# Optimization experiments

Measured on AMD Instinct MI355X. Metric: run time of the kernel, lower is better.

Reference implementation:

```python
import jax, jax.numpy as jnp
import numpy as np

B, C = 2, 128
FMAP_HW = [(256, 256), (128, 128), (64, 64), (32, 32)]
N_ROIS = 4000
POOL = (7, 7)
N_ANCH = 300000
N_POS = 1000          # anchors with match > 0 (class 1)
N_NEG = 200000        # anchors with match == -1
SHEM_POOLSIZE = 20
N_CLASSES = 2


def setup_inputs() -> dict:
    key = jax.random.key(0)
    ks = jax.random.split(key, 10)
    inp = {}
    for l, (h, w) in enumerate(FMAP_HW):
        inp[f"fmap{l}"] = jax.random.normal(ks[l], (B, C, h, w), dtype=jnp.float32)
    # rois: normalized (y1, x1, y2, x2, batch_ix)
    ctr = jax.random.uniform(ks[4], (N_ROIS, 2))
    sz = jax.random.uniform(ks[5], (N_ROIS, 2), minval=0.02, maxval=0.5)
    lo = jnp.clip(ctr - sz / 2, 0.0, 1.0)
    hi = jnp.clip(ctr + sz / 2, 0.0, 1.0)
    bix = jax.random.randint(ks[6], (N_ROIS, 1), 0, B).astype(jnp.float32)
    inp["rois"] = jnp.concatenate([lo, hi, bix], axis=1)
    # fixed layout for static shapes: [pos | neg | neutral]
    am = np.zeros(N_ANCH, np.int32)
    am[:N_POS] = 1
    am[N_POS:N_POS + N_NEG] = -1
    inp["anchor_matches"] = jnp.asarray(am)
    inp["class_pred_logits"] = jax.random.normal(ks[7], (N_ANCH, N_CLASSES), dtype=jnp.float32)
    inp["pred_deltas"] = jax.random.normal(ks[8], (N_ANCH, 4), dtype=jnp.float32) * 0.1
    inp["target_deltas"] = jax.random.normal(ks[9], (N_ANCH, 4), dtype=jnp.float32) * 0.1
    return inp


def _roi_align_2d(fmap, boxes, batch_ix, pool):
    """Bilinear ROI align, one sample at each bin center.
    fmap: [B,C,H,W]; boxes: [N,4] in fmap pixel coords (y1,x1,y2,x2).
    Returns [N,C,ph,pw]."""
    Hc, Wc = fmap.shape[2], fmap.shape[3]
    ph, pw = pool
    y1, x1, y2, x2 = boxes[:, 0], boxes[:, 1], boxes[:, 2], boxes[:, 3]
    bh = (y2 - y1) / ph
    bw = (x2 - x1) / pw
    iy = jnp.arange(ph, dtype=jnp.float32) + 0.5
    ix = jnp.arange(pw, dtype=jnp.float32) + 0.5
    sy = jnp.clip(y1[:, None] + bh[:, None] * iy[None, :], 0.0, Hc - 1.0)  # [N,ph]
    sx = jnp.clip(x1[:, None] + bw[:, None] * ix[None, :], 0.0, Wc - 1.0)  # [N,pw]
    y0f = jnp.floor(sy)
    x0f = jnp.floor(sx)
    y0 = y0f.astype(jnp.int32)
    x0 = x0f.astype(jnp.int32)
    y1i = jnp.minimum(y0 + 1, Hc - 1)
    x1i = jnp.minimum(x0 + 1, Wc - 1)
    wy = (sy - y0f)[:, :, None, None]  # [N,ph,1,1]
    wx = (sx - x0f)[:, None, :, None]  # [N,1,pw,1]
    b = batch_ix[:, None, None]

    def gather(yy, xx):
        # yy [N,ph], xx [N,pw] -> [N,ph,pw,C]
        return fmap[b, :, yy[:, :, None], xx[:, None, :]]

    v00 = gather(y0, x0)
    v01 = gather(y0, x1i)
    v10 = gather(y1i, x0)
    v11 = gather(y1i, x1i)
    out = (v00 * (1 - wy) * (1 - wx) + v01 * (1 - wy) * wx
           + v10 * wy * (1 - wx) + v11 * wy * wx)
    return jnp.transpose(out, (0, 3, 1, 2))


def _forward(fmaps, rois, anchor_matches, class_pred_logits, pred_deltas, target_deltas):
    boxes = rois[:, :4]
    batch_ix = rois[:, 4].astype(jnp.int32)
    h = boxes[:, 2] - boxes[:, 0]
    w = boxes[:, 3] - boxes[:, 1]
    roi_level = jnp.clip(
        jnp.round(4.0 + jnp.log2(jnp.sqrt(h * w + 1e-12))).astype(jnp.int32), 0, 3)
    boxes_sg = jax.lax.stop_gradient(boxes)  # original detaches level_boxes
    pooled = jnp.zeros((N_ROIS, C, POOL[0], POOL[1]), fmaps[0].dtype)
    for lvl, f in enumerate(fmaps):
        He, We = f.shape[2], f.shape[3]
        lb = boxes_sg * jnp.array([He, We, He, We], jnp.float32)
        pl = _roi_align_2d(f, lb, batch_ix, POOL)
        mask = (roi_level == lvl).astype(pl.dtype)[:, None, None, None]
        pooled = pooled + mask * pl  # each roi hits exactly one level; order preserved

    # ---- class loss with SHEM (layout: [:N_POS] pos, [N_POS:N_POS+N_NEG] neg) ----
    pos_logits = class_pred_logits[:N_POS]
    pos_targets = anchor_matches[:N_POS].astype(jnp.int32)
    pos_logp = jax.nn.log_softmax(pos_logits, axis=1)
    pos_loss = -jnp.mean(jnp.take_along_axis(pos_logp, pos_targets[:, None], axis=1))

    neg_logits = class_pred_logits[N_POS:N_POS + N_NEG]
    neg_bg_prob = jax.nn.softmax(neg_logits, axis=1)[:, 0]
    negative_count = N_POS  # max(1, n_pos)
    pool_n = min(negative_count * SHEM_POOLSIZE, N_NEG)
    order = jnp.argsort(neg_bg_prob)          # ascending bg prob = hardest first
    pool_idx = order[:pool_n]
    perm = jax.random.permutation(jax.random.key(1), pool_n)
    neg_ix = pool_idx[perm[:negative_count]]  # stochastic draw from hard pool
    neg_loss = -jnp.mean(jax.nn.log_softmax(neg_logits[neg_ix], axis=1)[:, 0])
    class_loss = (pos_loss + neg_loss) / 2.0

    # ---- bbox smooth-L1 on positives (beta=1, mean reduction) ----
    diff = jnp.abs(pred_deltas[:N_POS] - target_deltas[:N_POS])
    sl1 = jnp.where(diff < 1.0, 0.5 * diff * diff, diff - 0.5)
    bbox_loss = jnp.mean(sl1)
    return pooled, class_loss, bbox_loss


def reference(fmap0, fmap1, fmap2, fmap3, rois, anchor_matches,
              class_pred_logits, pred_deltas, target_deltas):
    return _forward([fmap0, fmap1, fmap2, fmap3], rois, anchor_matches,
                    class_pred_logits, pred_deltas, target_deltas)
```

## Files before the change

kernel.cpp:

```cpp
#include <hip/hip_runtime.h>
#include <hip/hip_bf16.h>
#include <cstdint>

#define NROIS  4000
#define NCH    128
#define NBINS  49
#define N_POSA 1000
#define N_NEGA 200000
#define POOLN  20000
#define HBITS_A 13
#define ABINS  8192
#define PBINS  4096
#define SUBN   4096
#define NTRBLK 2720
#define NPREP  106
#define NRANKA 512
#define NRANKP 40
#define TPAD   136

#define L0OFF 0ull
#define L1OFF 16777216ull
#define L2OFF 20971520ull
#define L3OFF 22020096ull
#define TLELEMS 22282240ull

__device__ __forceinline__ uint32_t rotl32d(uint32_t v, int r) { return (v << r) | (v >> (32-r)); }

__device__ void tf2x32(uint32_t k0, uint32_t k1, uint32_t& x0, uint32_t& x1)
{
    const uint32_t ks2 = k0 ^ k1 ^ 0x1BD11BDAu;
    const int R0[4] = {13,15,26,6};
    const int R1[4] = {17,29,16,24};
    x0 += k0; x1 += k1;
#pragma unroll
    for (int r = 0; r < 4; ++r) { x0 += x1; x1 = rotl32d(x1, R0[r]); x1 ^= x0; }
    x0 += k1;  x1 += ks2 + 1u;
#pragma unroll
    for (int r = 0; r < 4; ++r) { x0 += x1; x1 = rotl32d(x1, R1[r]); x1 ^= x0; }
    x0 += ks2; x1 += k0 + 2u;
#pragma unroll
    for (int r = 0; r < 4; ++r) { x0 += x1; x1 = rotl32d(x1, R0[r]); x1 ^= x0; }
    x0 += k0;  x1 += k1 + 3u;
#pragma unroll
    for (int r = 0; r < 4; ++r) { x0 += x1; x1 = rotl32d(x1, R1[r]); x1 ^= x0; }
    x0 += k1;  x1 += ks2 + 4u;
#pragma unroll
    for (int r = 0; r < 4; ++r) { x0 += x1; x1 = rotl32d(x1, R0[r]); x1 ^= x0; }
    x0 += ks2; x1 += k0 + 5u;
}

__device__ __forceinline__ unsigned int monobits(float x) {
    unsigned int u = __float_as_uint(x);
    return (u & 0x80000000u) ? ~u : (u | 0x80000000u);
}

__device__ __forceinline__ unsigned short f2bf(float x) {
    union { __hip_bfloat16 h; unsigned short u; } c;
    c.h = __float2bfloat16(x);
    return c.u;
}

__global__ void k_zero(unsigned int* __restrict__ h, unsigned int* __restrict__ rA,
                       unsigned int* __restrict__ rP1, unsigned int* __restrict__ rP2)
{
    const int b = blockIdx.x;
    const int i = b*256 + threadIdx.x;
    if      (b <  64) h[i] = 0u;
    else if (b <  96) rA[i - 64*256] = 0u;
    else if (b < 112) rP1[i - 96*256] = 0u;
    else              rP2[i - 112*256] = 0u;
}

__global__ __launch_bounds__(256) void k_trprep(
    const float* __restrict__ f0, const float* __restrict__ f1,
    const float* __restrict__ f2, const float* __restrict__ f3,
    __hip_bfloat16* __restrict__ tl,
    unsigned long long* __restrict__ T1, unsigned long long* __restrict__ T2,
    unsigned int* __restrict__ histA,
    unsigned int* __restrict__ histP1, unsigned int* __restrict__ histP2,
    const int* __restrict__ am, const float* __restrict__ logits,
    const float* __restrict__ pd, const float* __restrict__ td,
    float* __restrict__ prt, int ntr)
{
    __shared__ __align__(16) unsigned char smraw[32768];
    const int bid = blockIdx.x;
    const int t   = threadIdx.x;

    if (bid < ntr) {
        unsigned short* s = (unsigned short*)smraw;
        const int bz = bid / 1360;
        const int r  = bid - bz*1360;
        int lvl, tile;
        if      (r < 1024) { lvl = 0; tile = r; }
        else if (r < 1280) { lvl = 1; tile = r - 1024; }
        else if (r < 1344) { lvl = 2; tile = r - 1280; }
        else               { lvl = 3; tile = r - 1344; }
        const int HW = 65536 >> (2*lvl);
        const float* in = (lvl==0) ? f0 : (lvl==1) ? f1 : (lvl==2) ? f2 : f3;
        const size_t ooff = (lvl==0) ? L0OFF : (lvl==1) ? L1OFF : (lvl==2) ? L2OFF : L3OFF;
        const int hw0 = tile * 64;
        const float4* in4 = (const float4*)(in + (size_t)bz * 128 * HW);
        const int HW4 = HW >> 2;
        const int h4b = hw0 >> 2;
#pragma unroll
        for (int k = 0; k < 8; ++k) {
            const int idx = t + k*256;
            const int c   = idx >> 4;
            const int h4  = idx & 15;
            const float4 v = in4[(size_t)c * HW4 + h4b + h4];
            const int r0 = h4 * 4;
            const int cs = c ^ ((h4 & 7) << 3);
            s[(r0+0)*TPAD + cs] = f2bf(v.x);
            s[(r0+1)*TPAD + cs] = f2bf(v.y);
            s[(r0+2)*TPAD + cs] = f2bf(v.z);
            s[(r0+3)*TPAD + cs] = f2bf(v.w);
        }
        __syncthreads();
        uint4* out4 = (uint4*)(tl + ooff + (size_t)bz * (size_t)HW * 128
                                         + (size_t)hw0 * 128);
        const int rr = t >> 4;
        const int q  = t & 15;
        const int c8 = q * 8;
#pragma unroll
        for (int m = 0; m < 4; ++m) {
            const int row = rr + m*16;
            const int sw = ((row >> 2) & 7) << 3;
            out4[row*16 + q] = *(const uint4*)&s[row*TPAD + (c8 ^ sw)];
        }
        return;
    }

    const int pbid = bid - ntr;
    if (pbid < 40) {
        unsigned int* buf = (unsigned int*)smraw;
        unsigned int* lh1 = buf;
        unsigned int* lh2 = buf + PBINS;
        for (int b = t; b < 2*PBINS; b += 256) buf[b] = 0u;
        __syncthreads();
        const int i = pbid*256 + t;
        if (i < POOLN/2) {
            uint32_t a0 = 0u, a1 = 2u; tf2x32(0u, 1u, a0, a1);
            uint32_t b0 = 1u, b1 = 3u; tf2x32(0u, 1u, b0, b1);
            uint32_t c0 = 0u, c1 = 2u; tf2x32(a0, b0, c0, c1);
            uint32_t d0 = 1u, d1 = 3u; tf2x32(a0, b0, d0, d1);
            uint32_t x0 = (uint32_t)i, x1 = (uint32_t)(POOLN/2 + i);
            tf2x32(a1, b1, x0, x1);
            T1[i]           = ((unsigned long long)x0 << 32) | (unsigned)i;
            T1[POOLN/2 + i] = ((unsigned long long)x1 << 32) | (unsigned)(POOLN/2 + i);
            atomicAdd(&lh1[x0 >> 20], 1u);
            atomicAdd(&lh1[x1 >> 20], 1u);
            uint32_t y0 = (uint32_t)i, y1 = (uint32_t)(POOLN/2 + i);
            tf2x32(c1, d1, y0, y1);
            T2[i]           = ((unsigned long long)y0 << 32) | (unsigned)i;
            T2[POOLN/2 + i] = ((unsigned long long)y1 << 32) | (unsigned)(POOLN/2 + i);
            atomicAdd(&lh2[y0 >> 20], 1u);
            atomicAdd(&lh2[y1 >> 20], 1u);
        }
        __syncthreads();
        for (int b = t; b < PBINS; b += 256) {
            unsigned int v = lh1[b]; if (v) atomicAdd(&histP1[b], v);
            v = lh2[b];              if (v) atomicAdd(&histP2[b], v);
        }
        return;
    }
    if (pbid < 104) {
        unsigned int* buf = (unsigned int*)smraw;
        for (int b = t; b < ABINS; b += 256) buf[b] = 0u;
        __syncthreads();
        for (int i = (pbid-40)*256 + t; i < N_NEGA; i += 64*256) {
            const float l0 = logits[(size_t)(N_POSA+i)*2+0];
            const float l1 = logits[(size_t)(N_POSA+i)*2+1];
            atomicAdd(&buf[monobits(l0 - l1) >> (32-HBITS_A)], 1u);
        }
        __syncthreads();
        for (int b = t; b < ABINS; b += 256) {
            const unsigned int v = buf[b];
            if (v) atomicAdd(&histA[b], v);
        }
        return;
    }
    float* red = (float*)smraw;
    float s = 0.0f;
    if (pbid == 104) {
        for (int i = t; i < N_POSA; i += 256) {
            const int tgt = am[i];
            const float l0 = logits[(size_t)i*2+0], l1 = logits[(size_t)i*2+1];
            const float m = fmaxf(l0, l1);
            const float lse = logf(expf(l0-m) + expf(l1-m));
            const float lt = (tgt == 0) ? l0 : l1;
            s += (lt - m) - lse;
        }
    } else {
        for (int i = t; i < N_POSA*4; i += 256) {
            const float d = fabsf(pd[i] - td[i]);
            s += (d < 1.0f) ? 0.5f*d*d : d - 0.5f;
        }
    }
    red[t] = s;
    __syncthreads();
    for (int off = 128; off > 0; off >>= 1) {
        if (t < off) red[t] += red[t+off];
        __syncthreads();
    }
    if (t == 0) prt[pbid - 104] = red[0];
}

__device__ void scan_one256(const unsigned int* __restrict__ hist,
                            unsigned int* __restrict__ base, int n, unsigned int* lds)
{
    const int t = threadIdx.x;
    const int chunk = n >> 8;
    unsigned int s = 0;
    for (int k = 0; k < chunk; ++k) s += hist[t*chunk + k];
    lds[t] = s;
    __syncthreads();
    for (int off = 1; off < 256; off <<= 1) {
        unsigned int v = (t >= off) ? lds[t-off] : 0u;
        __syncthreads();
        lds[t] += v;
        __syncthreads();
    }
    unsigned int run = (t == 0) ? 0u : lds[t-1];
    for (int k = 0; k < chunk; ++k) {
        base[t*chunk+k] = run;
        run += hist[t*chunk+k];
    }
    if (t == 255) base[n] = run;
    __syncthreads();
}

__device__ void do_roi(int n, const __hip_bfloat16* __restrict__ tl,
                       const float* __restrict__ rois, float* __restrict__ out,
                       unsigned char* smraw)
{
    int   (*s_a)[4] = (int(*)[4])smraw;
    float (*s_w)[4] = (float(*)[4])(smraw + 784);
    float* s_o      = (float*)(smraw + 1568);
    const int tid = threadIdx.x;

    const float ry1 = rois[n*5+0], rx1 = rois[n*5+1];
    const float ry2 = rois[n*5+2], rx2 = rois[n*5+3];
    const int   b   = (int)rois[n*5+4];
    const float h = ry2 - ry1, w = rx2 - rx1;
    const float lraw = rintf(4.0f + log2f(sqrtf(h*w + 1e-12f)));
    int lvl = (int)lraw; lvl = lvl < 0 ? 0 : (lvl > 3 ? 3 : lvl);
    const int H = 256 >> lvl;
    const size_t lbase = (lvl==0) ? L0OFF : (lvl==1) ? L1OFF : (lvl==2) ? L2OFF : L3OFF;
    const __hip_bfloat16* bp = tl + lbase + (size_t)b * (size_t)(H*H) * NCH;

    const float Hf  = (float)H;
    const float y1p = ry1*Hf, x1p = rx1*Hf, y2p = ry2*Hf, x2p = rx2*Hf;
    const float bh = (y2p - y1p) / 7.0f, bw = (x2p - x1p) / 7.0f;

    if (tid < NBINS) {
        const int py = tid / 7, px = tid % 7;
        float sy = y1p + bh*((float)py + 0.5f);
        float sx = x1p + bw*((float)px + 0.5f);
        sy = fminf(fmaxf(sy, 0.0f), Hf - 1.0f);
        sx = fminf(fmaxf(sx, 0.0f), Hf - 1.0f);
        const float y0f = floorf(sy), x0f = floorf(sx);
        const int y0 = (int)y0f, x0 = (int)x0f;
        const int y1i = min(y0+1, H-1), x1i = min(x0+1, H-1);
        const float wy = sy - y0f, wx = sx - x0f;
        s_a[tid][0] = y0 *H + x0;
        s_a[tid][1] = y0 *H + x1i;
        s_a[tid][2] = y1i*H + x0;
        s_a[tid][3] = y1i*H + x1i;
        const float omy = 1.0f - wy, omx = 1.0f - wx;
        s_w[tid][0] = omy*omx; s_w[tid][1] = omy*wx;
        s_w[tid][2] = wy *omx; s_w[tid][3] = wy *wx;
    }
    __syncthreads();

    const int c8 = tid & 7;
    const int bg = tid >> 3;
#pragma unroll
    for (int half = 0; half < 2; ++half) {
        if (half) __syncthreads();
        for (int bin = bg; bin < NBINS; bin += 32) {
            float a0=0.f,a1=0.f,a2=0.f,a3=0.f,a4=0.f,a5=0.f,a6=0.f,a7=0.f;
#pragma unroll
            for (int tap = 0; tap < 4; ++tap) {
                const uint4 v = *(const uint4*)
                    (bp + (size_t)s_a[bin][tap]*NCH + half*64 + 8*c8);
                const float wgt = s_w[bin][tap];
                a0 += __uint_as_float(v.x << 16)         * wgt;
                a1 += __uint_as_float(v.x & 0xffff0000u) * wgt;
                a2 += __uint_as_float(v.y << 16)         * wgt;
                a3 += __uint_as_float(v.y & 0xffff0000u) * wgt;
                a4 += __uint_as_float(v.z << 16)         * wgt;
                a5 += __uint_as_float(v.z & 0xffff0000u) * wgt;
                a6 += __uint_as_float(v.w << 16)         * wgt;
                a7 += __uint_as_float(v.w & 0xffff0000u) * wgt;
            }
            s_o[(8*c8+0)*NBINS + bin] = a0;
            s_o[(8*c8+1)*NBINS + bin] = a1;
            s_o[(8*c8+2)*NBINS + bin] = a2;
            s_o[(8*c8+3)*NBINS + bin] = a3;
            s_o[(8*c8+4)*NBINS + bin] = a4;
            s_o[(8*c8+5)*NBINS + bin] = a5;
            s_o[(8*c8+6)*NBINS + bin] = a6;
            s_o[(8*c8+7)*NBINS + bin] = a7;
        }
        __syncthreads();
        float4* outn = (float4*)(out + (size_t)n*(NCH*NBINS) + half*64*NBINS);
        const float4* so4 = (const float4*)s_o;
        for (int t4 = tid; t4 < (64*NBINS)/4; t4 += 256)
            outn[t4] = so4[t4];
    }
}

__global__ __launch_bounds__(256, 8) void k_stage3(
    const __hip_bfloat16* __restrict__ tl, const float* __restrict__ rois,
    float* __restrict__ out, const float* __restrict__ logits,
    const unsigned long long* __restrict__ T1, const unsigned long long* __restrict__ T2,
    unsigned long long* __restrict__ A,
    unsigned long long* __restrict__ P1, unsigned long long* __restrict__ P2,
    const unsigned int* __restrict__ histA,
    const unsigned int* __restrict__ histP1, const unsigned int* __restrict__ histP2,
    unsigned int* __restrict__ baseA, unsigned int* __restrict__ baseP1,
    unsigned int* __restrict__ baseP2,
    unsigned int* __restrict__ resvA, unsigned int* __restrict__ resvP1,
    unsigned int* __restrict__ resvP2,
    unsigned int* __restrict__ sel, int rcnt)
{
    __shared__ __align__(16) unsigned char smraw[17440];
    const int bid = blockIdx.x;
    const int t   = threadIdx.x;
    if (bid < rcnt) { do_roi(bid, tl, rois, out, smraw); return; }

    const int sbid = bid - rcnt;
    if (sbid == 0) {
        unsigned int* lds = (unsigned int*)smraw;
        scan_one256(histA, baseA, ABINS, lds);
        scan_one256(histP1, baseP1, PBINS, lds);
        scan_one256(histP2, baseP2, PBINS, lds);
        const int chunk = ABINS >> 8;
        for (int k = 0; k < chunk; ++k) {
            const int bin = t*chunk + k;
            if (baseA[bin] < POOLN && baseA[bin] + histA[bin] >= POOLN)
                sel[0] = (unsigned int)bin;
        }
        return;
    }
    if (sbid <= 64) {
        const int sa = sbid - 1;
        unsigned int* lh   = (unsigned int*)smraw;
        unsigned int* temp = (unsigned int*)(smraw + 16384);
        unsigned int* svl  = (unsigned int*)(smraw + 17408);
        for (int b = t; b < ABINS/2; b += 256) lh[b] = 0u;
        unsigned int s = 0;
        for (int k = 0; k < 32; ++k) s += histA[t*32 + k];
        temp[t] = s;
        __syncthreads();
        for (int off = 1; off < 256; off <<= 1) {
            const unsigned int v = (t >= off) ? temp[t-off] : 0u;
            __syncthreads();
            temp[t] += v;
            __syncthreads();
        }
        unsigned int run = (t == 0) ? 0u : temp[t-1];
        for (int k = 0; k < 32; ++k) {
            const int b = t*32 + k;
            const unsigned int hv = histA[b];
            if (run < POOLN && run + hv >= POOLN) svl[0] = (unsigned int)b;
            run += hv;
        }
        __syncthreads();
        const unsigned int selv = svl[0];
        const int start = sa * (N_NEGA/64);
        const int end   = start + (N_NEGA/64);
        for (int i = start + t; i < end; i += 256) {
            const float l0 = logits[(size_t)(N_POSA+i)*2+0];
            const float l1 = logits[(size_t)(N_POSA+i)*2+1];
            const unsigned int bin = monobits(l0 - l1) >> (32-HBITS_A);
            if (bin <= selv) atomicAdd(&lh[bin >> 1], 1u << ((bin & 1) << 4));
        }
        __syncthreads();
        run = (t == 0) ? 0u : temp[t-1];
        for (int k = 0; k < 32; k += 2) {
            const int b0 = t*32 + k;
            const unsigned int packed = lh[b0 >> 1];
            const unsigned int c0 = packed & 0xFFFFu, c1 = packed >> 16;
            unsigned int n0 = 0u, n1 = 0u;
// ... 17 lines not shown
            }
        }
        return;
    }
    {
        const int sp = sbid - 65;
        unsigned short* b1   = (unsigned short*)smraw;
        unsigned short* b2   = (unsigned short*)(smraw + 8192);
        unsigned int*   temp = (unsigned int*)(smraw + 16384);
        unsigned int s = 0;
        for (int k = 0; k < 16; ++k) s += histP1[t*16 + k];
        temp[t] = s;
        __syncthreads();
        for (int off = 1; off < 256; off <<= 1) {
            const unsigned int v = (t >= off) ? temp[t-off] : 0u;
            __syncthreads(); temp[t] += v; __syncthreads();
        }
        unsigned int run = (t == 0) ? 0u : temp[t-1];
        for (int k = 0; k < 16; ++k) {
            const int b = t*16 + k;
            b1[b] = (unsigned short)run;
            run += histP1[b];
        }
        __syncthreads();
        s = 0;
        for (int k = 0; k < 16; ++k) s += histP2[t*16 + k];
        temp[t] = s;
        __syncthreads();
        for (int off = 1; off < 256; off <<= 1) {
            const unsigned int v = (t >= off) ? temp[t-off] : 0u;
            __syncthreads(); temp[t] += v; __syncthreads();
        }
        run = (t == 0) ? 0u : temp[t-1];
        for (int k = 0; k < 16; ++k) {
            const int b = t*16 + k;
            b2[b] = (unsigned short)run;
            run += histP2[b];
        }
        __syncthreads();
        const int i = sp*256 + t;
        if (i < POOLN) {
            const unsigned long long k1 = T1[i];
            const unsigned int bn1 = (unsigned)(k1 >> 52);
            const unsigned int p1 = (unsigned)b1[bn1] + atomicAdd(&resvP1[bn1], 1u);
            P1[p1] = k1;
            const unsigned long long k2 = T2[i];
            const unsigned int bn2 = (unsigned)(k2 >> 52);
            const unsigned int p2 = (unsigned)b2[bn2] + atomicAdd(&resvP2[bn2], 1u);
            P2[p2] = k2;
        }
    }
}

__global__ __launch_bounds__(256) void k_roi(
    const float* __restrict__ f0, const float* __restrict__ f1,
    const float* __restrict__ f2, const float* __restrict__ f3,
    const float* __restrict__ rois, float* __restrict__ out)
{
    __shared__ int   s_a[NBINS][4];
    __shared__ float s_w[NBINS][4];
    const int n   = blockIdx.x;
    const int tid = threadIdx.x;

    const float ry1 = rois[n*5+0], rx1 = rois[n*5+1];
    const float ry2 = rois[n*5+2], rx2 = rois[n*5+3];
    const int   b   = (int)rois[n*5+4];
    const float h = ry2 - ry1, w = rx2 - rx1;
    const float lraw = rintf(4.0f + log2f(sqrtf(h*w + 1e-12f)));
    int lvl = (int)lraw; lvl = lvl < 0 ? 0 : (lvl > 3 ? 3 : lvl);
    const int H = 256 >> lvl;
    const float* f = (lvl==0) ? f0 : (lvl==1) ? f1 : (lvl==2) ? f2 : f3;

    const float Hf  = (float)H;
    const float y1p = ry1*Hf, x1p = rx1*Hf, y2p = ry2*Hf, x2p = rx2*Hf;
    const float bh = (y2p - y1p) / 7.0f, bw = (x2p - x1p) / 7.0f;

    if (tid < NBINS) {
        const int py = tid / 7, px = tid % 7;
        float sy = y1p + bh*((float)py + 0.5f);
        float sx = x1p + bw*((float)px + 0.5f);
        sy = fminf(fmaxf(sy, 0.0f), Hf - 1.0f);
        sx = fminf(fmaxf(sx, 0.0f), Hf - 1.0f);
        const float y0f = floorf(sy), x0f = floorf(sx);
        const int y0 = (int)y0f, x0 = (int)x0f;
        const int y1i = min(y0+1, H-1), x1i = min(x0+1, H-1);
        const float wy = sy - y0f, wx = sx - x0f;
        s_a[tid][0] = y0 *H + x0;
        s_a[tid][1] = y0 *H + x1i;
        s_a[tid][2] = y1i*H + x0;
        s_a[tid][3] = y1i*H + x1i;
        const float omy = 1.0f - wy, omx = 1.0f - wx;
        s_w[tid][0] = omy*omx; s_w[tid][1] = omy*wx;
        s_w[tid][2] = wy *omx; s_w[tid][3] = wy *wx;
    }
    __syncthreads();

    const int hw = H*H;
    const float* basep = f + (size_t)b * NCH * hw;
    float* outn = out + (size_t)n * (NCH*NBINS);
    for (int t = tid; t < NCH*NBINS; t += 256) {
        const int c   = t / NBINS;
        const int bin = t - c*NBINS;
        const float* p = basep + (size_t)c * hw;
        outn[t] = p[s_a[bin][0]]*s_w[bin][0] + p[s_a[bin][1]]*s_w[bin][1]
                + p[s_a[bin][2]]*s_w[bin][2] + p[s_a[bin][3]]*s_w[bin][3];
    }
}

__global__ __launch_bounds__(1024) void k_rank(
    const unsigned long long* __restrict__ A,
    const unsigned long long* __restrict__ P1, const unsigned long long* __restrict__ P2,
    const unsigned int* __restrict__ baseA,
    const unsigned int* __restrict__ baseP1, const unsigned int* __restrict__ baseP2,
    const unsigned int* __restrict__ sel,
    unsigned int* __restrict__ As, unsigned int* __restrict__ P1s,
    unsigned int* __restrict__ P2s)
{
    __shared__ unsigned long long g[SUBN];
    __shared__ unsigned int h2[SUBN];
    __shared__ unsigned int h2b[SUBN];
    const int bid = blockIdx.x;
    const int t   = threadIdx.x;
    if (bid < NRANKA) {
        const unsigned int selv = sel[0];
        for (unsigned int bin = (unsigned)bid; bin <= selv; bin += NRANKA) {
            const int base = (int)baseA[bin];
            const int cnt  = (int)baseA[bin+1] - base;
            if (cnt <= 0) continue;
            if (cnt == 1) {
                if (t == 0) As[base] = (unsigned)(A[base] & 0xffffffffu);
                continue;
            }
            if (cnt <= SUBN) {
                for (int b = t; b < SUBN; b += 1024) h2[b] = 0u;
                __syncthreads();
                for (int k = t; k < cnt; k += 1024) {
                    const unsigned int sub = ((unsigned)(A[base+k] >> 32) >> 7) & (SUBN-1);
                    atomicAdd(&h2[sub], 1u);
                }
                __syncthreads();
                unsigned int c0 = h2[4*t+0], c1 = h2[4*t+1],
                             c2 = h2[4*t+2], c3 = h2[4*t+3];
                h2b[t] = c0 + c1 + c2 + c3;
                __syncthreads();
                for (int off = 1; off < 1024; off <<= 1) {
                    const unsigned int v = (t >= off) ? h2b[t-off] : 0u;
                    __syncthreads();
                    h2b[t] += v;
                    __syncthreads();
                }
                unsigned int run = (t == 0) ? 0u : h2b[t-1];
                __syncthreads();
                h2[4*t+0] = run; h2b[4*t+0] = run; run += c0;
                h2[4*t+1] = run; h2b[4*t+1] = run; run += c1;
                h2[4*t+2] = run; h2b[4*t+2] = run; run += c2;
                h2[4*t+3] = run; h2b[4*t+3] = run; run += c3;
                __syncthreads();
                for (int k = t; k < cnt; k += 1024) {
                    const unsigned long long key = A[base+k];
                    const unsigned int sub = ((unsigned)(key >> 32) >> 7) & (SUBN-1);
                    const unsigned int p = atomicAdd(&h2[sub], 1u);
                    g[p] = key;
                }
                __syncthreads();
                for (int p = t; p < cnt; p += 1024) {
                    const unsigned long long key = g[p];
                    const unsigned int sub = ((unsigned)(key >> 32) >> 7) & (SUBN-1);
                    const int b0 = (int)h2b[sub], e0 = (int)h2[sub];
                    int r = b0;
                    for (int q = b0; q < e0; ++q) r += (g[q] < key) ? 1 : 0;
                    As[base + r] = (unsigned)(key & 0xffffffffu);
                }
                __syncthreads();
            } else {
                for (int k = t; k < cnt; k += 1024) {
                    const unsigned long long key = A[base+k];
                    int rank = 0;
                    for (int j = 0; j < cnt; ++j) rank += (A[base+j] < key) ? 1 : 0;
                    As[base + rank] = (unsigned)(key & 0xffffffffu);
                }
            }
        }
        return;
    }
    const int gg = (bid - NRANKA)*1024 + t;
    if (gg < POOLN) {
        const unsigned long long key = P1[gg];
        const unsigned int bin = (unsigned)(key >> 52);
        const int b0 = (int)baseP1[bin], b1 = (int)baseP1[bin+1];
        int rank = 0;
        for (int j = b0; j < b1; ++j) rank += (P1[j] < key) ? 1 : 0;
        P1s[b0 + rank] = (unsigned)(key & 0xffffffffu);
    } else if (gg < 2*POOLN) {
        const int e = gg - POOLN;
        const unsigned long long key = P2[e];
        const unsigned int bin = (unsigned)(key >> 52);
        const int b0 = (int)baseP2[bin], b1 = (int)baseP2[bin+1];
        int rank = 0;
        for (int j = b0; j < b1; ++j) rank += (P2[j] < key) ? 1 : 0;
        P2s[b0 + rank] = (unsigned)(key & 0xffffffffu);
    }
}

__global__ __launch_bounds__(256) void k_final(
    const float* __restrict__ logits, const unsigned int* __restrict__ As,
    const unsigned int* __restrict__ P1s, const unsigned int* __restrict__ P2s,
    const float* __restrict__ partial, float* __restrict__ out2)
{
    __shared__ float red[256];
    const int t = threadIdx.x;
    float s = 0.0f;
    for (int j = t; j < N_POSA; j += 256) {
        const unsigned int i2 = P2s[j];
        const unsigned int r  = P1s[i2];
        const unsigned int i  = As[r];
        const float l0 = logits[(size_t)(N_POSA+i)*2+0];
        const float l1 = logits[(size_t)(N_POSA+i)*2+1];
        const float m = fmaxf(l0, l1);
        s += (l0 - m) - logf(expf(l0-m) + expf(l1-m));
    }
    red[t] = s;
    __syncthreads();
    for (int off = 128; off > 0; off >>= 1) {
        if (t < off) red[t] += red[t+off];
        __syncthreads();
    }
    if (t == 0) {
        const float neg_loss = -red[0] / (float)N_POSA;
        const float pos_loss = -partial[0] / (float)N_POSA;
        out2[0] = 0.5f * (pos_loss + neg_loss);
        out2[1] = partial[1] / (float)(N_POSA*4);
    }
}

extern "C" void kernel_launch(void* const* d_in, const int* in_sizes, int n_in,
                              void* d_out, int out_size, void* d_ws, size_t ws_size,
                              hipStream_t stream)
{
    const float* f0     = (const float*)d_in[0];
    const float* f1     = (const float*)d_in[1];
    const float* f2     = (const float*)d_in[2];
    const float* f3     = (const float*)d_in[3];
    const float* rois   = (const float*)d_in[4];
    const int*   am     = (const int*)  d_in[5];
    const float* logits = (const float*)d_in[6];
    const float* pd     = (const float*)d_in[7];
    const float* td     = (const float*)d_in[8];
    float* out = (float*)d_out;

    char* ws = (char*)d_ws;
    unsigned long long* A      = (unsigned long long*)(ws);
    unsigned long long* T1     = (unsigned long long*)(ws +  262144);
    unsigned long long* T2     = (unsigned long long*)(ws +  422144);
    unsigned long long* P1     = (unsigned long long*)(ws +  582144);
    unsigned long long* P2     = (unsigned long long*)(ws +  742144);
    unsigned int*       histA  = (unsigned int*)      (ws +  902144);
    unsigned int*       histP1 = (unsigned int*)      (ws +  934912);
    unsigned int*       histP2 = (unsigned int*)      (ws +  951296);
    unsigned int*       baseA  = (unsigned int*)      (ws +  967680);
    unsigned int*       resvA  = (unsigned int*)      (ws + 1000512);
    unsigned int*       baseP1 = (unsigned int*)      (ws + 1033344);
    unsigned int*       resvP1 = (unsigned int*)      (ws + 1049792);
    unsigned int*       baseP2 = (unsigned int*)      (ws + 1066240);
    unsigned int*       resvP2 = (unsigned int*)      (ws + 1082688);
    unsigned int*       sel    = (unsigned int*)      (ws + 1099136);
    float*              prt    = (float*)             (ws + 1099200);
    __hip_bfloat16*     tl     = (__hip_bfloat16*)    (ws + 1099264);
    unsigned int*       As     = (unsigned int*)T1;
    unsigned int*       P1s    = (unsigned int*)T2;
    unsigned int*       P2s    = (unsigned int*)((char*)T2 + 80000);
    const size_t NEED = 1099264ull + TLELEMS * 2ull;
    const bool use_cl = (ws_size >= NEED);
    const int rcnt = use_cl ? NROIS : 0;

    k_zero<<<128, 256, 0, stream>>>(histA, resvA, resvP1, resvP2);

    k_trprep<<<(use_cl ? NTRBLK : 0) + NPREP, 256, 0, stream>>>(
        f0, f1, f2, f3, tl, T1, T2, histA, histP1, histP2,
        am, logits, pd, td, prt, use_cl ? NTRBLK : 0);

    if (!use_cl)
        k_roi<<<NROIS, 256, 0, stream>>>(f0, f1, f2, f3, rois, out);

    k_stage3<<<rcnt + 144, 256, 0, stream>>>(tl, rois, out, logits,
                                             T1, T2, A, P1, P2,
                                             histA, histP1, histP2,
                                             baseA, baseP1, baseP2,
                                             resvA, resvP1, resvP2, sel, rcnt);

    k_rank<<<NRANKA + NRANKP, 1024, 0, stream>>>(A, P1, P2, baseA, baseP1, baseP2,
                                                 sel, As, P1s, P2s);

    k_final<<<1, 256, 0, stream>>>(logits, As, P1s, P2s, prt,
                                   out + (size_t)NROIS*NCH*NBINS);
}
```

Measured before the change: 98.13 us.

## Split transpose by level and overlap ROI align with rank stages

The feature-map transpose is split: levels 1-3 are transposed in the first stage and level 0 in the second stage. ROIs are bucketed by pyramid level so level-1..3 ROIs run alongside the level-0 transpose, and level-0 ROIs run in the final rank stage alongside sorting. The rank kernel moves from 1024-thread to 256-thread blocks, and shared-memory histograms are packed into 16-bit halves. The intent is to fill idle GPU time across kernel boundaries, at the cost of atomics for list building, more scheduling complexity and a risk of 16-bit counter overflow in the packed histograms.

```diff
diff --git a/kernel.cpp b/kernel.cpp
--- a/kernel.cpp
+++ b/kernel.cpp
@@ -12,11 +12,12 @@
 #define ABINS  8192
 #define PBINS  4096
 #define SUBN   4096
-#define NTRBLK 2720
-#define NPREP  106
+#define NPREP  107
 #define NRANKA 512
-#define NRANKP 40
+#define NRANKP 157
 #define TPAD   136
+#define NTRA   672
+#define NTRB   2048
 
 #define L0OFF 0ull
 #define L1OFF 16777216ull
@@ -60,8 +61,17 @@
     return c.u;
 }
 
+__device__ __forceinline__ int roi_level(const float* __restrict__ rois, int n)
+{
+    const float h = rois[n*5+2] - rois[n*5+0];
+    const float w = rois[n*5+3] - rois[n*5+1];
+    const float lraw = rintf(4.0f + log2f(sqrtf(h*w + 1e-12f)));
+    int lvl = (int)lraw; return lvl < 0 ? 0 : (lvl > 3 ? 3 : lvl);
+}
+
 __global__ void k_zero(unsigned int* __restrict__ h, unsigned int* __restrict__ rA,
-                       unsigned int* __restrict__ rP1, unsigned int* __restrict__ rP2)
+                       unsigned int* __restrict__ rP1, unsigned int* __restrict__ rP2,
+                       unsigned int* __restrict__ cnt)
 {
     const int b = blockIdx.x;
     const int i = b*256 + threadIdx.x;
@@ -69,164 +79,55 @@
     else if (b <  96) rA[i - 64*256] = 0u;
     else if (b < 112) rP1[i - 96*256] = 0u;
     else              rP2[i - 112*256] = 0u;
-}
-
-__global__ __launch_bounds__(256) void k_trprep(
-    const float* __restrict__ f0, const float* __restrict__ f1,
-    const float* __restrict__ f2, const float* __restrict__ f3,
-    __hip_bfloat16* __restrict__ tl,
-    unsigned long long* __restrict__ T1, unsigned long long* __restrict__ T2,
-    unsigned int* __restrict__ histA,
-    unsigned int* __restrict__ histP1, unsigned int* __restrict__ histP2,
-    const int* __restrict__ am, const float* __restrict__ logits,
-    const float* __restrict__ pd, const float* __restrict__ td,
-    float* __restrict__ prt, int ntr)
-{
-    __shared__ __align__(16) unsigned char smraw[32768];
-    const int bid = blockIdx.x;
-    const int t   = threadIdx.x;
-
-    if (bid < ntr) {
-        unsigned short* s = (unsigned short*)smraw;
-        const int bz = bid / 1360;
-        const int r  = bid - bz*1360;
-        int lvl, tile;
-        if      (r < 1024) { lvl = 0; tile = r; }
-        else if (r < 1280) { lvl = 1; tile = r - 1024; }
-        else if (r < 1344) { lvl = 2; tile = r - 1280; }
-        else               { lvl = 3; tile = r - 1344; }
-        const int HW = 65536 >> (2*lvl);
-        const float* in = (lvl==0) ? f0 : (lvl==1) ? f1 : (lvl==2) ? f2 : f3;
-        const size_t ooff = (lvl==0) ? L0OFF : (lvl==1) ? L1OFF : (lvl==2) ? L2OFF : L3OFF;
-        const int hw0 = tile * 64;
-        const float4* in4 = (const float4*)(in + (size_t)bz * 128 * HW);
-        const int HW4 = HW >> 2;
-        const int h4b = hw0 >> 2;
-#pragma unroll
-        for (int k = 0; k < 8; ++k) {
-            const int idx = t + k*256;
-            const int c   = idx >> 4;
-            const int h4  = idx & 15;
-            const float4 v = in4[(size_t)c * HW4 + h4b + h4];
-            const int r0 = h4 * 4;
-            const int cs = c ^ ((h4 & 7) << 3);
-            s[(r0+0)*TPAD + cs] = f2bf(v.x);
-            s[(r0+1)*TPAD + cs] = f2bf(v.y);
-            s[(r0+2)*TPAD + cs] = f2bf(v.z);
-            s[(r0+3)*TPAD + cs] = f2bf(v.w);
-        }
-        __syncthreads();
-        uint4* out4 = (uint4*)(tl + ooff + (size_t)bz * (size_t)HW * 128
-                                         + (size_t)hw0 * 128);
-        const int rr = t >> 4;
-        const int q  = t & 15;
-        const int c8 = q * 8;
-#pragma unroll
-        for (int m = 0; m < 4; ++m) {
-            const int row = rr + m*16;
-            const int sw = ((row >> 2) & 7) << 3;
-            out4[row*16 + q] = *(const uint4*)&s[row*TPAD + (c8 ^ sw)];
-        }
-        return;
-    }
-
-    const int pbid = bid - ntr;
-    if (pbid < 40) {
-        unsigned int* buf = (unsigned int*)smraw;
-        unsigned int* lh1 = buf;
-        unsigned int* lh2 = buf + PBINS;
-        for (int b = t; b < 2*PBINS; b += 256) buf[b] = 0u;
-        __syncthreads();
-        const int i = pbid*256 + t;
-        if (i < POOLN/2) {
-            uint32_t a0 = 0u, a1 = 2u; tf2x32(0u, 1u, a0, a1);
-            uint32_t b0 = 1u, b1 = 3u; tf2x32(0u, 1u, b0, b1);
-            uint32_t c0 = 0u, c1 = 2u; tf2x32(a0, b0, c0, c1);
-            uint32_t d0 = 1u, d1 = 3u; tf2x32(a0, b0, d0, d1);
-            uint32_t x0 = (uint32_t)i, x1 = (uint32_t)(POOLN/2 + i);
-            tf2x32(a1, b1, x0, x1);
-            T1[i]           = ((unsigned long long)x0 << 32) | (unsigned)i;
-            T1[POOLN/2 + i] = ((unsigned long long)x1 << 32) | (unsigned)(POOLN/2 + i);
-            atomicAdd(&lh1[x0 >> 20], 1u);
-            atomicAdd(&lh1[x1 >> 20], 1u);
-            uint32_t y0 = (uint32_t)i, y1 = (uint32_t)(POOLN/2 + i);
-            tf2x32(c1, d1, y0, y1);
-            T2[i]           = ((unsigned long long)y0 << 32) | (unsigned)i;
-            T2[POOLN/2 + i] = ((unsigned long long)y1 << 32) | (unsigned)(POOLN/2 + i);
-            atomicAdd(&lh2[y0 >> 20], 1u);
-            atomicAdd(&lh2[y1 >> 20], 1u);
-        }
-        __syncthreads();
-        for (int b = t; b < PBINS; b += 256) {
-            unsigned int v = lh1[b]; if (v) atomicAdd(&histP1[b], v);
-            v = lh2[b];              if (v) atomicAdd(&histP2[b], v);
-        }
-        return;
-    }
-    if (pbid < 104) {
-        unsigned int* buf = (unsigned int*)smraw;
-        for (int b = t; b < ABINS; b += 256) buf[b] = 0u;
-        __syncthreads();
-        for (int i = (pbid-40)*256 + t; i < N_NEGA; i += 64*256) {
-            const float l0 = logits[(size_t)(N_POSA+i)*2+0];
-            const float l1 = logits[(size_t)(N_POSA+i)*2+1];
-            atomicAdd(&buf[monobits(l0 - l1) >> (32-HBITS_A)], 1u);
-        }
-        __syncthreads();
-        for (int b = t; b < ABINS; b += 256) {
-            const unsigned int v = buf[b];
-            if (v) atomicAdd(&histA[b], v);
-        }
-        return;
-    }
-    float* red = (float*)smraw;
-    float s = 0.0f;
-    if (pbid == 104) {
-        for (int i = t; i < N_POSA; i += 256) {
-            const int tgt = am[i];
-            const float l0 = logits[(size_t)i*2+0], l1 = logits[(size_t)i*2+1];
-            const float m = fmaxf(l0, l1);
-            const float lse = logf(expf(l0-m) + expf(l1-m));
-            const float lt = (tgt == 0) ? l0 : l1;
-            s += (lt - m) - lse;
-        }
-    } else {
-        for (int i = t; i < N_POSA*4; i += 256) {
-            const float d = fabsf(pd[i] - td[i]);
-            s += (d < 1.0f) ? 0.5f*d*d : d - 0.5f;
-        }
-    }
-    red[t] = s;
+    if (b == 0 && threadIdx.x < 2) cnt[threadIdx.x] = 0u;
+}
+
+__device__ void do_transpose(int trid, const float* __restrict__ f0,
+                             const float* __restrict__ f1, const float* __restrict__ f2,
+                             const float* __restrict__ f3,
+                             __hip_bfloat16* __restrict__ tl, unsigned char* smraw)
+{
+    unsigned short* s = (unsigned short*)smraw;
+    const int t  = threadIdx.x;
+    const int bz = trid / 1360;
+    const int r  = trid - bz*1360;
+    int lvl, tile;
+    if      (r < 1024) { lvl = 0; tile = r; }
+    else if (r < 1280) { lvl = 1; tile = r - 1024; }
+    else if (r < 1344) { lvl = 2; tile = r - 1280; }
+    else               { lvl = 3; tile = r - 1344; }
+    const int HW = 65536 >> (2*lvl);
+    const float* in = (lvl==0) ? f0 : (lvl==1) ? f1 : (lvl==2) ? f2 : f3;
+    const size_t ooff = (lvl==0) ? L0OFF : (lvl==1) ? L1OFF : (lvl==2) ? L2OFF : L3OFF;
+    const int hw0 = tile * 64;
+    const float4* in4 = (const float4*)(in + (size_t)bz * 128 * HW);
+    const int HW4 = HW >> 2;
+    const int h4b = hw0 >> 2;
+#pragma unroll
+    for (int k = 0; k < 8; ++k) {
+        const int idx = t + k*256;
+        const int c   = idx >> 4;
+        const int h4  = idx & 15;
+        const float4 v = in4[(size_t)c * HW4 + h4b + h4];
+        const int r0 = h4 * 4;
+        const int cs = c ^ ((h4 & 7) << 3);
+        s[(r0+0)*TPAD + cs] = f2bf(v.x);
+        s[(r0+1)*TPAD + cs] = f2bf(v.y);
+        s[(r0+2)*TPAD + cs] = f2bf(v.z);
+        s[(r0+3)*TPAD + cs] = f2bf(v.w);
+    }
     __syncthreads();
-    for (int off = 128; off > 0; off >>= 1) {
-        if (t < off) red[t] += red[t+off];
-        __syncthreads();
-    }
-    if (t == 0) prt[pbid - 104] = red[0];
-}
-
-__device__ void scan_one256(const unsigned int* __restrict__ hist,
-                            unsigned int* __restrict__ base, int n, unsigned int* lds)
-{
-    const int t = threadIdx.x;
-    const int chunk = n >> 8;
-    unsigned int s = 0;
-    for (int k = 0; k < chunk; ++k) s += hist[t*chunk + k];
-    lds[t] = s;
-    __syncthreads();
-    for (int off = 1; off < 256; off <<= 1) {
-        unsigned int v = (t >= off) ? lds[t-off] : 0u;
-        __syncthreads();
-        lds[t] += v;
-        __syncthreads();
-    }
-    unsigned int run = (t == 0) ? 0u : lds[t-1];
-    for (int k = 0; k < chunk; ++k) {
-        base[t*chunk+k] = run;
-        run += hist[t*chunk+k];
-    }
-    if (t == 255) base[n] = run;
-    __syncthreads();
+    uint4* out4 = (uint4*)(tl + ooff + (size_t)bz * (size_t)HW * 128
+                                     + (size_t)hw0 * 128);
+    const int rr = t >> 4;
+    const int q  = t & 15;
+    const int c8 = q * 8;
+#pragma unroll
+    for (int m = 0; m < 4; ++m) {
+        const int row = rr + m*16;
+        const int sw = ((row >> 2) & 7) << 3;
+        out4[row*16 + q] = *(const uint4*)&s[row*TPAD + (c8 ^ sw)];
+    }
 }
 
 __device__ void do_roi(int n, const __hip_bfloat16* __restrict__ tl,
@@ -241,9 +142,7 @@
     const float ry1 = rois[n*5+0], rx1 = rois[n*5+1];
     const float ry2 = rois[n*5+2], rx2 = rois[n*5+3];
     const int   b   = (int)rois[n*5+4];
-    const float h = ry2 - ry1, w = rx2 - rx1;
-    const float lraw = rintf(4.0f + log2f(sqrtf(h*w + 1e-12f)));
-    int lvl = (int)lraw; lvl = lvl < 0 ? 0 : (lvl > 3 ? 3 : lvl);
+    const int lvl = roi_level(rois, n);
     const int H = 256 >> lvl;
     const size_t lbase = (lvl==0) ? L0OFF : (lvl==1) ? L1OFF : (lvl==2) ? L2OFF : L3OFF;
     const __hip_bfloat16* bp = tl + lbase + (size_t)b * (size_t)(H*H) * NCH;
@@ -310,8 +209,143 @@
     }
 }
 
-__global__ __launch_bounds__(256, 8) void k_stage3(
-    const __hip_bfloat16* __restrict__ tl, const float* __restrict__ rois,
+__global__ __launch_bounds__(256) void k_stageA(
+    const float* __restrict__ f0, const float* __restrict__ f1,
+    const float* __restrict__ f2, const float* __restrict__ f3,
+    __hip_bfloat16* __restrict__ tl, const float* __restrict__ rois,
+    unsigned long long* __restrict__ T1, unsigned long long* __restrict__ T2,
+    unsigned int* __restrict__ histA,
+    unsigned int* __restrict__ histP1, unsigned int* __restrict__ histP2,
+    const int* __restrict__ am, const float* __restrict__ logits,
+    const float* __restrict__ pd, const float* __restrict__ td,
+    float* __restrict__ prt,
+    unsigned int* __restrict__ listHi, unsigned int* __restrict__ listLo,
+    unsigned int* __restrict__ cnt, int ntrA)
+{
+    __shared__ __align__(16) unsigned char smraw[17408];
+    const int bid = blockIdx.x;
+    const int t   = threadIdx.x;
+
+    if (bid < ntrA) {
+        const int bz = bid / 336;
+        const int rr = 1024 + (bid - bz*336);
+        do_transpose(bz*1360 + rr, f0, f1, f2, f3, tl, smraw);
+        return;
+    }
+
+    const int pbid = bid - ntrA;
+    if (pbid < 40) {
+        unsigned int* buf = (unsigned int*)smraw;
+        unsigned int* lh = buf;
+        for (int b = t; b < PBINS; b += 256) lh[b] = 0u;
+        __syncthreads();
+        const int i = pbid*256 + t;
+        if (i < POOLN/2) {
+            uint32_t a0 = 0u, a1 = 2u; tf2x32(0u, 1u, a0, a1);
+            uint32_t b0 = 1u, b1 = 3u; tf2x32(0u, 1u, b0, b1);
+            uint32_t c0 = 0u, c1 = 2u; tf2x32(a0, b0, c0, c1);
+            uint32_t d0 = 1u, d1 = 3u; tf2x32(a0, b0, d0, d1);
+            uint32_t x0 = (uint32_t)i, x1 = (uint32_t)(POOLN/2 + i);
+            tf2x32(a1, b1, x0, x1);
+            T1[i]           = ((unsigned long long)x0 << 32) | (unsigned)i;
+            T1[POOLN/2 + i] = ((unsigned long long)x1 << 32) | (unsigned)(POOLN/2 + i);
+            atomicAdd(&lh[x0 >> 20], 1u);
+            atomicAdd(&lh[x1 >> 20], 1u);
+            uint32_t y0 = (uint32_t)i, y1 = (uint32_t)(POOLN/2 + i);
+            tf2x32(c1, d1, y0, y1);
+            T2[i]           = ((unsigned long long)y0 << 32) | (unsigned)i;
+            T2[POOLN/2 + i] = ((unsigned long long)y1 << 32) | (unsigned)(POOLN/2 + i);
+            atomicAdd(&lh[y0 >> 20], 0x10000u);
+            atomicAdd(&lh[y1 >> 20], 0x10000u);
+        }
+        __syncthreads();
+        for (int b = t; b < PBINS; b += 256) {
+            const unsigned int v = lh[b];
+            if (v & 0xFFFFu)  atomicAdd(&histP1[b], v & 0xFFFFu);
+            if (v >> 16)      atomicAdd(&histP2[b], v >> 16);
+        }
+        return;
+    }
+    if (pbid < 104) {
+        unsigned int* buf = (unsigned int*)smraw;
+        for (int b = t; b < ABINS/2; b += 256) buf[b] = 0u;
+        __syncthreads();
+        for (int i = (pbid-40)*256 + t; i < N_NEGA; i += 64*256) {
+            const float l0 = logits[(size_t)(N_POSA+i)*2+0];
+            const float l1 = logits[(size_t)(N_POSA+i)*2+1];
+            const unsigned int bin = monobits(l0 - l1) >> (32-HBITS_A);
+            atomicAdd(&buf[bin >> 1], 1u << ((bin & 1) << 4));
+        }
+        __syncthreads();
+        for (int b = t; b < ABINS/2; b += 256) {
+            const unsigned int v = buf[b];
+            if (v & 0xFFFFu) atomicAdd(&histA[2*b],   v & 0xFFFFu);
+            if (v >> 16)     atomicAdd(&histA[2*b+1], v >> 16);
+        }
+        return;
+    }
+    if (pbid == 106) {
+        for (int i = t; i < NROIS; i += 256) {
+            const int lvl = roi_level(rois, i);
+            if (lvl == 0) listLo[atomicAdd(&cnt[1], 1u)] = (unsigned)i;
+            else          listHi[atomicAdd(&cnt[0], 1u)] = (unsigned)i;
+        }
+        return;
+    }
+    float* red = (float*)smraw;
+    float s = 0.0f;
+    if (pbid == 104) {
+        for (int i = t; i < N_POSA; i += 256) {
+            const int tgt = am[i];
+            const float l0 = logits[(size_t)i*2+0], l1 = logits[(size_t)i*2+1];
+            const float m = fmaxf(l0, l1);
+            const float lse = logf(expf(l0-m) + expf(l1-m));
+            const float lt = (tgt == 0) ? l0 : l1;
+            s += (lt - m) - lse;
+        }
+    } else {
+        for (int i = t; i < N_POSA*4; i += 256) {
+            const float d = fabsf(pd[i] - td[i]);
+            s += (d < 1.0f) ? 0.5f*d*d : d - 0.5f;
+        }
+    }
+    red[t] = s;
+    __syncthreads();
+    for (int off = 128; off > 0; off >>= 1) {
+        if (t < off) red[t] += red[t+off];
+        __syncthreads();
+    }
+    if (t == 0) prt[pbid - 104] = red[0];
+}
+
+__device__ void scan_one256(const unsigned int* __restrict__ hist,
+                            unsigned int* __restrict__ base, int n, unsigned int* lds)
+{
+    const int t = threadIdx.x;
+    const int chunk = n >> 8;
+    unsigned int s = 0;
+    for (int k = 0; k < chunk; ++k) s += hist[t*chunk + k];
+    lds[t] = s;
+    __syncthreads();
+    for (int off = 1; off < 256; off <<= 1) {
+        unsigned int v = (t >= off) ? lds[t-off] : 0u;
+        __syncthreads();
+        lds[t] += v;
+        __syncthreads();
+    }
+    unsigned int run = (t == 0) ? 0u : lds[t-1];
+    for (int k = 0; k < chunk; ++k) {
+        base[t*chunk+k] = run;
+        run += hist[t*chunk+k];
+    }
+    if (t == 255) base[n] = run;
+    __syncthreads();
+}
+
+__global__ __launch_bounds__(256, 8) void k_stageB(
+    const float* __restrict__ f0, const float* __restrict__ f1,
+    const float* __restrict__ f2, const float* __restrict__ f3,
+    __hip_bfloat16* __restrict__ tl, const float* __restrict__ rois,
     float* __restrict__ out, const float* __restrict__ logits,
     const unsigned long long* __restrict__ T1, const unsigned long long* __restrict__ T2,
     unsigned long long* __restrict__ A,
@@ -322,14 +356,25 @@
     unsigned int* __restrict__ baseP2,
     unsigned int* __restrict__ resvA, unsigned int* __restrict__ resvP1,
     unsigned int* __restrict__ resvP2,
-    unsigned int* __restrict__ sel, int rcnt)
+    unsigned int* __restrict__ sel,
+    const unsigned int* __restrict__ listHi, const unsigned int* __restrict__ cnt,
+    int ntrB, int nslots)
 {
     __shared__ __align__(16) unsigned char smraw[17440];
     const int bid = blockIdx.x;
     const int t   = threadIdx.x;
-    if (bid < rcnt) { do_roi(bid, tl, rois, out, smraw); return; }
-
-    const int sbid = bid - rcnt;
+
+    if (bid < ntrB) {
+        const int bz = bid >> 10;
+        do_transpose(bz*1360 + (bid & 1023), f0, f1, f2, f3, tl, smraw);
+        return;
+    }
+    const int rid = bid - ntrB;
+    if (rid < nslots) {
+        if ((unsigned)rid < cnt[0]) do_roi((int)listHi[rid], tl, rois, out, smraw);
+        return;
+    }
+    const int sbid = rid - nslots;
     if (sbid == 0) {
         unsigned int* lds = (unsigned int*)smraw;
         scan_one256(histA, baseA, ABINS, lds);
@@ -453,6 +498,125 @@
     }
 }
 
+__global__ __launch_bounds__(256) void k_stageC(
+    const __hip_bfloat16* __restrict__ tl, const float* __restrict__ rois,
+    float* __restrict__ out,
+    const unsigned long long* __restrict__ A,
+    const unsigned long long* __restrict__ P1, const unsigned long long* __restrict__ P2,
+    const unsigned int* __restrict__ baseA,
+    const unsigned int* __restrict__ baseP1, const unsigned int* __restrict__ baseP2,
+    const unsigned int* __restrict__ sel,
+    unsigned int* __restrict__ As, unsigned int* __restrict__ P1s,
+    unsigned int* __restrict__ P2s,
+    const unsigned int* __restrict__ listLo, const unsigned int* __restrict__ cnt,
+    int nslots)
+{
+    __shared__ __align__(16) unsigned char smraw[32768];
+    const int bid = blockIdx.x;
+    const int t   = threadIdx.x;
+    if (bid < nslots) {
+        if ((unsigned)bid < cnt[1]) do_roi((int)listLo[bid], tl, rois, out, smraw);
+        return;
+    }
+    const int sbid = bid - nslots;
+    if (sbid < NRANKA) {
+        unsigned int*   gkey = (unsigned int*)smraw;
+        unsigned short* gsub = (unsigned short*)(smraw + 16384);
+        unsigned int*   h2p  = (unsigned int*)(smraw + 24576);
+        unsigned int*   st   = (unsigned int*)(smraw + 16384);
+        const unsigned int selv = sel[0];
+        for (unsigned int bin = (unsigned)sbid; bin <= selv; bin += NRANKA) {
+            const int base = (int)baseA[bin];
+            const int cnt_ = (int)baseA[bin+1] - base;
+            if (cnt_ <= 0) continue;
+            if (cnt_ == 1) {
+                if (t == 0) As[base] = (unsigned)(A[base] & 0xffffffffu);
+                continue;
+            }
+            if (cnt_ <= SUBN) {
+                for (int b = t; b < SUBN/2; b += 256) h2p[b] = 0u;
+                __syncthreads();
+                for (int k = t; k < cnt_; k += 256) {
+                    const unsigned int sub =
+                        ((unsigned)(A[base+k] >> 32) >> 7) & (SUBN-1);
+                    atomicAdd(&h2p[sub >> 1], 1u << ((sub & 1) << 4));
+                }
+                __syncthreads();
+                unsigned int tmp[8];
+                unsigned int s = 0;
+                for (int w = 0; w < 8; ++w) {
+                    const unsigned int v = h2p[t*8 + w];
+                    tmp[w] = v;
+                    s += (v & 0xFFFFu) + (v >> 16);
+                }
+                st[t] = s;
+                __syncthreads();
+                for (int off = 1; off < 256; off <<= 1) {
+                    const unsigned int v = (t >= off) ? st[t-off] : 0u;
+                    __syncthreads();
+                    st[t] += v;
+                    __syncthreads();
+                }
+                unsigned int run = (t == 0) ? 0u : st[t-1];
+                __syncthreads();
+                for (int w = 0; w < 8; ++w) {
+                    const unsigned int v = tmp[w];
+                    const unsigned int lo = run; run += (v & 0xFFFFu);
+                    const unsigned int hi = run; run += (v >> 16);
+                    h2p[t*8 + w] = lo | (hi << 16);
+                }
+                __syncthreads();
+                for (int k = t; k < cnt_; k += 256) {
+                    const unsigned long long key = A[base+k];
+                    const unsigned int bits = (unsigned)(key >> 32);
+                    const unsigned int sub  = (bits >> 7) & (SUBN-1);
+                    const unsigned int sh   = (sub & 1) << 4;
+                    const unsigned int old  = atomicAdd(&h2p[sub >> 1], 1u << sh);
+                    const unsigned int pos  = (old >> sh) & 0xFFFFu;
+                    gkey[pos] = ((bits & 0x7Fu) << 18) | (unsigned)(key & 0xffffffffu);
+                    gsub[pos] = (unsigned short)sub;
+                }
+                __syncthreads();
+                for (int p = t; p < cnt_; p += 256) {
+                    const unsigned int k25 = gkey[p];
+                    const unsigned short sb = gsub[p];
+                    int b0 = p; while (b0 > 0 && gsub[b0-1] == sb) --b0;
+                    int e0 = p; while (e0+1 < cnt_ && gsub[e0+1] == sb) ++e0;
+                    int r = b0;
+                    for (int q = b0; q <= e0; ++q) r += (gkey[q] < k25) ? 1 : 0;
+                    As[base + r] = k25 & 0x3FFFFu;
+                }
+                __syncthreads();
+            } else {
+                for (int k = t; k < cnt_; k += 256) {
+                    const unsigned long long key = A[base+k];
+                    int rank = 0;
+                    for (int j = 0; j < cnt_; ++j) rank += (A[base+j] < key) ? 1 : 0;
+                    As[base + rank] = (unsigned)(key & 0xffffffffu);
+                }
+            }
+        }
+        return;
+    }
+    const int g = (sbid - NRANKA)*256 + t;
+    if (g < POOLN) {
+        const unsigned long long key = P1[g];
+        const unsigned int bin = (unsigned)(key >> 52);
+        const int b0 = (int)baseP1[bin], b1 = (int)baseP1[bin+1];
+        int rank = 0;
+        for (int j = b0; j < b1; ++j) rank += (P1[j] < key) ? 1 : 0;
+        P1s[b0 + rank] = (unsigned)(key & 0xffffffffu);
+    } else if (g < 2*POOLN) {
+        const int e = g - POOLN;
+        const unsigned long long key = P2[e];
+        const unsigned int bin = (unsigned)(key >> 52);
+        const int b0 = (int)baseP2[bin], b1 = (int)baseP2[bin+1];
+        int rank = 0;
+        for (int j = b0; j < b1; ++j) rank += (P2[j] < key) ? 1 : 0;
+        P2s[b0 + rank] = (unsigned)(key & 0xffffffffu);
+    }
+}
+
 __global__ __launch_bounds__(256) void k_roi(
     const float* __restrict__ f0, const float* __restrict__ f1,
     const float* __restrict__ f2, const float* __restrict__ f3,
@@ -466,9 +630,7 @@
     const float ry1 = rois[n*5+0], rx1 = rois[n*5+1];
     const float ry2 = rois[n*5+2], rx2 = rois[n*5+3];
     const int   b   = (int)rois[n*5+4];
-    const float h = ry2 - ry1, w = rx2 - rx1;
-    const float lraw = rintf(4.0f + log2f(sqrtf(h*w + 1e-12f)));
-    int lvl = (int)lraw; lvl = lvl < 0 ? 0 : (lvl > 3 ? 3 : lvl);
+    const int lvl = roi_level(rois, n);
     const int H = 256 >> lvl;
     const float* f = (lvl==0) ? f0 : (lvl==1) ? f1 : (lvl==2) ? f2 : f3;
 
@@ -508,101 +670,6 @@
     }
 }
 
-__global__ __launch_bounds__(1024) void k_rank(
-    const unsigned long long* __restrict__ A,
-    const unsigned long long* __restrict__ P1, const unsigned long long* __restrict__ P2,
-    const unsigned int* __restrict__ baseA,
-    const unsigned int* __restrict__ baseP1, const unsigned int* __restrict__ baseP2,
-    const unsigned int* __restrict__ sel,
-    unsigned int* __restrict__ As, unsigned int* __restrict__ P1s,
-    unsigned int* __restrict__ P2s)
-{
-    __shared__ unsigned long long g[SUBN];
-    __shared__ unsigned int h2[SUBN];
-    __shared__ unsigned int h2b[SUBN];
-    const int bid = blockIdx.x;
-    const int t   = threadIdx.x;
-    if (bid < NRANKA) {
-        const unsigned int selv = sel[0];
-        for (unsigned int bin = (unsigned)bid; bin <= selv; bin += NRANKA) {
-            const int base = (int)baseA[bin];
-            const int cnt  = (int)baseA[bin+1] - base;
-            if (cnt <= 0) continue;
-            if (cnt == 1) {
-                if (t == 0) As[base] = (unsigned)(A[base] & 0xffffffffu);
-                continue;
-            }
-            if (cnt <= SUBN) {
-                for (int b = t; b < SUBN; b += 1024) h2[b] = 0u;
-                __syncthreads();
-                for (int k = t; k < cnt; k += 1024) {
-                    const unsigned int sub = ((unsigned)(A[base+k] >> 32) >> 7) & (SUBN-1);
-                    atomicAdd(&h2[sub], 1u);
-                }
-                __syncthreads();
-                unsigned int c0 = h2[4*t+0], c1 = h2[4*t+1],
-                             c2 = h2[4*t+2], c3 = h2[4*t+3];
-                h2b[t] = c0 + c1 + c2 + c3;
-                __syncthreads();
-                for (int off = 1; off < 1024; off <<= 1) {
-                    const unsigned int v = (t >= off) ? h2b[t-off] : 0u;
-                    __syncthreads();
-                    h2b[t] += v;
-                    __syncthreads();
-                }
-                unsigned int run = (t == 0) ? 0u : h2b[t-1];
-                __syncthreads();
-                h2[4*t+0] = run; h2b[4*t+0] = run; run += c0;
-                h2[4*t+1] = run; h2b[4*t+1] = run; run += c1;
-                h2[4*t+2] = run; h2b[4*t+2] = run; run += c2;
-                h2[4*t+3] = run; h2b[4*t+3] = run; run += c3;
-                __syncthreads();
-                for (int k = t; k < cnt; k += 1024) {
-                    const unsigned long long key = A[base+k];
-                    const unsigned int sub = ((unsigned)(key >> 32) >> 7) & (SUBN-1);
-                    const unsigned int p = atomicAdd(&h2[sub], 1u);
-                    g[p] = key;
-                }
-                __syncthreads();
-                for (int p = t; p < cnt; p += 1024) {
-                    const unsigned long long key = g[p];
-                    const unsigned int sub = ((unsigned)(key >> 32) >> 7) & (SUBN-1);
-                    const int b0 = (int)h2b[sub], e0 = (int)h2[sub];
-                    int r = b0;
-                    for (int q = b0; q < e0; ++q) r += (g[q] < key) ? 1 : 0;
-                    As[base + r] = (unsigned)(key & 0xffffffffu);
-                }
-                __syncthreads();
-            } else {
-                for (int k = t; k < cnt; k += 1024) {
-                    const unsigned long long key = A[base+k];
-                    int rank = 0;
-                    for (int j = 0; j < cnt; ++j) rank += (A[base+j] < key) ? 1 : 0;
-                    As[base + rank] = (unsigned)(key & 0xffffffffu);
-                }
-            }
-        }
-        return;
-    }
-    const int gg = (bid - NRANKA)*1024 + t;
-    if (gg < POOLN) {
-        const unsigned long long key = P1[gg];
-        const unsigned int bin = (unsigned)(key >> 52);
-        const int b0 = (int)baseP1[bin], b1 = (int)baseP1[bin+1];
-        int rank = 0;
-        for (int j = b0; j < b1; ++j) rank += (P1[j] < key) ? 1 : 0;
-        P1s[b0 + rank] = (unsigned)(key & 0xffffffffu);
-    } else if (gg < 2*POOLN) {
-        const int e = gg - POOLN;
-        const unsigned long long key = P2[e];
-        const unsigned int bin = (unsigned)(key >> 52);
-        const int b0 = (int)baseP2[bin], b1 = (int)baseP2[bin+1];
-        int rank = 0;
-        for (int j = b0; j < b1; ++j) rank += (P2[j] < key) ? 1 : 0;
-        P2s[b0 + rank] = (unsigned)(key & 0xffffffffu);
-    }
-}
-
 __global__ __launch_bounds__(256) void k_final(
     const float* __restrict__ logits, const unsigned int* __restrict__ As,
     const unsigned int* __restrict__ P1s, const unsigned int* __restrict__ P2s,
@@ -666,31 +733,40 @@
     unsigned int*       resvP2 = (unsigned int*)      (ws + 1082688);
     unsigned int*       sel    = (unsigned int*)      (ws + 1099136);
     float*              prt    = (float*)             (ws + 1099200);
-    __hip_bfloat16*     tl     = (__hip_bfloat16*)    (ws + 1099264);
+    unsigned int*       listHi = (unsigned int*)      (ws + 1099264);
+    unsigned int*       listLo = (unsigned int*)      (ws + 1115264);
+    unsigned int*       cnt    = (unsigned int*)      (ws + 1131264);
+    __hip_bfloat16*     tl     = (__hip_bfloat16*)    (ws + 1131328);
     unsigned int*       As     = (unsigned int*)T1;
     unsigned int*       P1s    = (unsigned int*)T2;
     unsigned int*       P2s    = (unsigned int*)((char*)T2 + 80000);
-    const size_t NEED = 1099264ull + TLELEMS * 2ull;
+    const size_t NEED = 1131328ull + TLELEMS * 2ull;
     const bool use_cl = (ws_size >= NEED);
-    const int rcnt = use_cl ? NROIS : 0;
-
-    k_zero<<<128, 256, 0, stream>>>(histA, resvA, resvP1, resvP2);
-
-    k_trprep<<<(use_cl ? NTRBLK : 0) + NPREP, 256, 0, stream>>>(
-        f0, f1, f2, f3, tl, T1, T2, histA, histP1, histP2,
-        am, logits, pd, td, prt, use_cl ? NTRBLK : 0);
+
+    k_zero<<<128, 256, 0, stream>>>(histA, resvA, resvP1, resvP2, cnt);
+
+    k_stageA<<<(use_cl ? NTRA : 0) + NPREP, 256, 0, stream>>>(
+        f0, f1, f2, f3, tl, rois, T1, T2, histA, histP1, histP2,
+        am, logits, pd, td, prt, listHi, listLo, cnt, use_cl ? NTRA : 0);
 
     if (!use_cl)
         k_roi<<<NROIS, 256, 0, stream>>>(f0, f1, f2, f3, rois, out);
 
-    k_stage3<<<rcnt + 144, 256, 0, stream>>>(tl, rois, out, logits,
-                                             T1, T2, A, P1, P2,
-                                             histA, histP1, histP2,
-                                             baseA, baseP1, baseP2,
-                                             resvA, resvP1, resvP2, sel, rcnt);
-
-    k_rank<<<NRANKA + NRANKP, 1024, 0, stream>>>(A, P1, P2, baseA, baseP1, baseP2,
-                                                 sel, As, P1s, P2s);
+    {
+        const int ntrB   = use_cl ? NTRB : 0;
+        const int nslots = use_cl ? NROIS : 0;
+        k_stageB<<<ntrB + nslots + 144, 256, 0, stream>>>(
+            f0, f1, f2, f3, tl, rois, out, logits, T1, T2, A, P1, P2,
+            histA, histP1, histP2, baseA, baseP1, baseP2,
+            resvA, resvP1, resvP2, sel, listHi, cnt, ntrB, nslots);
+    }
+
+    {
+        const int nslots = use_cl ? NROIS : 0;
+        k_stageC<<<nslots + NRANKA + NRANKP, 256, 0, stream>>>(
+            tl, rois, out, A, P1, P2, baseA, baseP1, baseP2, sel,
+            As, P1s, P2s, listLo, cnt, nslots);
+    }
 
     k_final<<<1, 256, 0, stream>>>(logits, As, P1s, P2s, prt,
                                    out + (size_t)NROIS*NCH*NBINS);
```

Measured after the change: 173.6 us. 76.9% more time.
